# Kernel tuning notes

Measured on AMD Instinct MI355X. Metric: run time of the kernel, lower is better.

Reference implementation:

```python
import jax, jax.numpy as jnp
import numpy as np

N_NODES = 100000
N_EDGES = 1600000
IN_DIM, HID_DIM, OUT_DIM = 128, 64, 64


def setup_inputs() -> dict:
    key = jax.random.key(0)
    ks = jax.random.split(key, 12)
    x = jax.random.normal(ks[0], (N_NODES, IN_DIM), dtype=jnp.float32)
    src = jax.random.randint(ks[1], (N_EDGES,), 0, N_NODES, dtype=jnp.int32)
    dst = jax.random.randint(ks[2], (N_EDGES,), 0, N_NODES, dtype=jnp.int32)
    def glorot(k, shape):
        lim = float(np.sqrt(6.0 / (shape[0] + shape[1])))
        return jax.random.uniform(k, shape, jnp.float32, -lim, lim)
    W0 = glorot(ks[3], (IN_DIM, HID_DIM)); b0 = jnp.zeros((HID_DIM,), jnp.float32)
    W1 = glorot(ks[4], (HID_DIM, HID_DIM)); b1 = jnp.zeros((HID_DIM,), jnp.float32)
    W2 = glorot(ks[5], (HID_DIM, OUT_DIM)); b2 = jnp.zeros((OUT_DIM,), jnp.float32)
    Wl = glorot(ks[6], (OUT_DIM, OUT_DIM)); bl = jnp.zeros((OUT_DIM,), jnp.float32)
    return {"x": x, "src": src, "dst": dst,
            "W0": W0, "b0": b0, "W1": W1, "b1": b1,
            "W2": W2, "b2": b2, "Wl": Wl, "bl": bl}


def _graph_conv(x, src, dst, W, b, inv_sqrt_out, inv_sqrt_in):
    # DGL GraphConv, norm='both': D_out^{-1/2} then XW, SpMM aggregate, D_in^{-1/2}, +bias
    h = x * inv_sqrt_out[:, None]          # [N, d_in]
    h = h @ W                               # [N, d_out] (project first: d_in >= d_out)
    agg = jax.ops.segment_sum(h[src], dst, num_segments=N_NODES)  # gather+scatter over edges
    return agg * inv_sqrt_in[:, None] + b


def reference(x, src, dst, W0, b0, W1, b1, W2, b2, Wl, bl):
    ones_e = jnp.ones((N_EDGES,), jnp.float32)
    deg_out = jnp.clip(jax.ops.segment_sum(ones_e, src, num_segments=N_NODES), 1.0)
    deg_in = jnp.clip(jax.ops.segment_sum(ones_e, dst, num_segments=N_NODES), 1.0)
    inv_out = jax.lax.rsqrt(deg_out)
    inv_in = jax.lax.rsqrt(deg_in)
    h = jax.nn.elu(_graph_conv(x, src, dst, W0, b0, inv_out, inv_in))
    h = jax.nn.elu(_graph_conv(h, src, dst, W1, b1, inv_out, inv_in))
    h = _graph_conv(h, src, dst, W2, b2, inv_out, inv_in)
    return jax.nn.elu(h) @ Wl + bl
```

## Files before the change

kernel.cpp:

```cpp
#include <hip/hip_runtime.h>
#include <hip/hip_fp16.h>
#include <cstdint>
#include <cstddef>


#define WG 256
static constexpr int NCHUNK = 512;
static constexpr int RW_SH  = 7;
static constexpr int RWID   = 1 << RW_SH;
static constexpr int BPRO   = 12512;
static constexpr int NRO    = 8;
static constexpr int NCO    = 40;

typedef _Float16 half8 __attribute__((ext_vector_type(8)));
typedef _Float16 half2v __attribute__((ext_vector_type(2)));
typedef float f32x4 __attribute__((ext_vector_type(4)));

__device__ __forceinline__ int block_scan_excl(int v, int tid, int* sd, int& total) {
  sd[tid] = v;
  __syncthreads();
  for (int off = 1; off < 256; off <<= 1) {
    int t = (tid >= off) ? sd[tid - off] : 0;
    __syncthreads();
    sd[tid] += t;
    __syncthreads();
  }
  int incl = sd[tid];
  total = sd[255];
  __syncthreads();
  return incl - v;
}

__global__ __launch_bounds__(WG) void coarse_hist_kernel(const int* __restrict__ dst,
                                                         int* __restrict__ cntA,
                                                         int NR, int E, int EPC) {
  __shared__ int cnt[1024];
  const int c = blockIdx.x, tid = threadIdx.x;
  for (int i = tid; i < NR; i += WG) cnt[i] = 0;
  __syncthreads();
  const int base = c * EPC;
  const int nv4 = EPC >> 2;
  const int4* d4 = (const int4*)(dst + base);
  for (int i = tid; i < nv4; i += WG) {
    const int e = base + (i << 2);
    if (e + 3 < E) {
      const int4 v = d4[i];
      atomicAdd(&cnt[v.x >> RW_SH], 1);
      atomicAdd(&cnt[v.y >> RW_SH], 1);
      atomicAdd(&cnt[v.z >> RW_SH], 1);
      atomicAdd(&cnt[v.w >> RW_SH], 1);
    } else {
      for (int j = 0; j < 4; ++j) {
        const int ee = e + j;
        if (ee < E) atomicAdd(&cnt[dst[ee] >> RW_SH], 1);
      }
    }
  }
  __syncthreads();
  for (int i = tid; i < NR; i += WG) cntA[i * NCHUNK + c] = cnt[i];
}

__global__ __launch_bounds__(WG) void chunkscan_kernel(const int* __restrict__ cntA,
                                                       int* __restrict__ base_rel,
                                                       int* __restrict__ cntR) {
  __shared__ int sd[256];
  const int r = blockIdx.x, tid = threadIdx.x;
  const int row = r * NCHUNK;
  int t0, t1;
  const int v0 = cntA[row + tid];
  const int e0 = block_scan_excl(v0, tid, sd, t0);
  base_rel[row + tid] = e0;
  const int v1 = cntA[row + 256 + tid];
  const int e1 = block_scan_excl(v1, tid, sd, t1);
  base_rel[row + 256 + tid] = t0 + e1;
  if (tid == 0) cntR[r] = t0 + t1;
}

__global__ __launch_bounds__(WG) void rangescan_kernel(const int* __restrict__ cntR,
                                                       int* __restrict__ rangeStart,
                                                       int* __restrict__ rptr,
                                                       int NR, int N, int E) {
  __shared__ int sd[256];
  const int tid = threadIdx.x;
  int carry = 0;
  for (int base = 0; base < NR; base += 256) {
    const int idx = base + tid;
    const int v = (idx < NR) ? cntR[idx] : 0;
    int tot;
    const int e = block_scan_excl(v, tid, sd, tot);
    if (idx < NR) rangeStart[idx] = carry + e;
    carry += tot;
  }
  if (tid == 0) { rangeStart[NR] = E; rptr[N] = E; }
}

__global__ __launch_bounds__(WG) void bucket_kernel(const int* __restrict__ src,
                                                    const int* __restrict__ dst,
                                                    const int* __restrict__ base_rel,
                                                    const int* __restrict__ rangeStart,
                                                    int* __restrict__ bucket,
                                                    int NR, int E, int EPC) {
  __shared__ int cur[1024];
  const int c = blockIdx.x, tid = threadIdx.x;
  for (int i = tid; i < NR; i += WG) cur[i] = rangeStart[i] + base_rel[i * NCHUNK + c];
  __syncthreads();
  const int base = c * EPC;
  const int nv4 = EPC >> 2;
  const int4* s4 = (const int4*)(src + base);
  const int4* d4 = (const int4*)(dst + base);
  for (int i = tid; i < nv4; i += WG) {
    const int e = base + (i << 2);
    if (e + 3 < E) {
      const int4 sv = s4[i];
      const int4 dv = d4[i];
      int p;
      p = atomicAdd(&cur[dv.x >> RW_SH], 1); bucket[p] = (sv.x << RW_SH) | (dv.x & (RWID - 1));
      p = atomicAdd(&cur[dv.y >> RW_SH], 1); bucket[p] = (sv.y << RW_SH) | (dv.y & (RWID - 1));
      p = atomicAdd(&cur[dv.z >> RW_SH], 1); bucket[p] = (sv.z << RW_SH) | (dv.z & (RWID - 1));
      p = atomicAdd(&cur[dv.w >> RW_SH], 1); bucket[p] = (sv.w << RW_SH) | (dv.w & (RWID - 1));
    } else {
      for (int j = 0; j < 4; ++j) {
        const int ee = e + j;
        if (ee < E) {
          const int s = src[ee], d = dst[ee];
          const int p = atomicAdd(&cur[d >> RW_SH], 1);
          bucket[p] = (s << RW_SH) | (d & (RWID - 1));
        }
      }
    }
  }
}

__global__ __launch_bounds__(WG) void csr_kernel(const int* __restrict__ bucket,
                                                 const int* __restrict__ rangeStart,
                                                 int* __restrict__ rptr,
                                                 int* __restrict__ degi,
                                                 int* __restrict__ esrc, int N) {
  __shared__ int hist[RWID], sd[256];
  const int r = blockIdx.x, tid = threadIdx.x;
  const int s0 = rangeStart[r], s1 = rangeStart[r + 1];
  if (tid < RWID) hist[tid] = 0;
  __syncthreads();
  for (int e = s0 + tid; e < s1; e += WG) atomicAdd(&hist[bucket[e] & (RWID - 1)], 1);
  __syncthreads();
  const int v = (tid < RWID) ? hist[tid] : 0;
  int tot;
  const int excl = block_scan_excl(v, tid, sd, tot);
  const int node = (r << RW_SH) + tid;
  if (tid < RWID && node < N) { degi[node] = v; rptr[node] = s0 + excl; }
  if (tid < RWID) hist[tid] = s0 + excl;
  __syncthreads();
  for (int e = s0 + tid; e < s1; e += WG) {
    const int pk = bucket[e];
    const int p = atomicAdd(&hist[pk & (RWID - 1)], 1);
    esrc[p] = pk >> RW_SH;
  }
}

__global__ __launch_bounds__(WG) void dego_hist_kernel(const int* __restrict__ src,
                                                       int* __restrict__ slab,
                                                       int N, int E, int EPCO) {
  __shared__ int h[BPRO / 2];
  const int rr = blockIdx.x / NCO, cc = blockIdx.x % NCO;
  const int tid = threadIdx.x;
  for (int i = tid; i < (BPRO >> 3); i += WG) ((int4*)h)[i] = make_int4(0, 0, 0, 0);
  __syncthreads();
  const int lo = rr * BPRO;
  const int base = cc * EPCO;
  const int nv4 = EPCO >> 2;
  const int4* s4 = (const int4*)(src + base);
  for (int i = tid; i < nv4; i += WG) {
    const int e = base + (i << 2);
    if (e + 3 < E) {
      const int4 v = s4[i];
      unsigned b;
      b = (unsigned)(v.x - lo); if (b < (unsigned)BPRO) atomicAdd((unsigned*)&h[b >> 1], 1u << ((b & 1) << 4));
      b = (unsigned)(v.y - lo); if (b < (unsigned)BPRO) atomicAdd((unsigned*)&h[b >> 1], 1u << ((b & 1) << 4));
      b = (unsigned)(v.z - lo); if (b < (unsigned)BPRO) atomicAdd((unsigned*)&h[b >> 1], 1u << ((b & 1) << 4));
      b = (unsigned)(v.w - lo); if (b < (unsigned)BPRO) atomicAdd((unsigned*)&h[b >> 1], 1u << ((b & 1) << 4));
    } else {
      for (int j = 0; j < 4; ++j) {
        const int ee = e + j;
        if (ee < E) {
          const unsigned b = (unsigned)(src[ee] - lo);
          if (b < (unsigned)BPRO) atomicAdd((unsigned*)&h[b >> 1], 1u << ((b & 1) << 4));
        }
      }
    }
  }
  __syncthreads();
  const int NW = N >> 1;
  const int wbase = lo >> 1;
  int* srow = slab + (size_t)cc * NW;
  for (int i = tid; i < (BPRO >> 3); i += WG) {
    const int wg = wbase + (i << 2);
    if (wg + 3 < NW) {
      ((int4*)(srow + wg))[0] = ((const int4*)h)[i];
    } else {
      for (int j = 0; j < 4; ++j)
        if (wg + j < NW) srow[wg + j] = h[(i << 2) + j];
    }
  }
}

__global__ __launch_bounds__(WG) void dego_reduce_inv_kernel(const int* __restrict__ slab,
                                                             const int* __restrict__ degi,
                                                             float* __restrict__ invo,
                                                             float* __restrict__ invi, int N) {
  const int NW = N >> 1;
  const int i = blockIdx.x * WG + threadIdx.x;
  if (i >= NW) return;
  unsigned s = 0;
#pragma unroll
  for (int c = 0; c < NCO; ++c) s += (unsigned)slab[(size_t)c * NW + i];
  int d0 = (int)(s & 0xffffu); if (d0 < 1) d0 = 1;
  int d1 = (int)(s >> 16);     if (d1 < 1) d1 = 1;
  const int2 dd = *(const int2*)(degi + 2 * i);
  const int i0 = (dd.x < 1) ? 1 : dd.x;
  const int i1 = (dd.y < 1) ? 1 : dd.y;
  *(float2*)(invo + 2 * i) = make_float2(rsqrtf((float)d0), rsqrtf((float)d1));
  *(float2*)(invi + 2 * i) = make_float2(rsqrtf((float)i0), rsqrtf((float)i1));
}

__global__ __launch_bounds__(WG) void wtrans_kernel(const float* __restrict__ W0,
                                                    const float* __restrict__ W1,
                                                    const float* __restrict__ W2,
                                                    const float* __restrict__ Wl,
                                                    _Float16* __restrict__ T0,
                                                    _Float16* __restrict__ T1,
                                                    _Float16* __restrict__ T2,
                                                    _Float16* __restrict__ Tl) {
  const float* W; _Float16* T; int K;
  switch (blockIdx.x) {
    case 0: W = W0; T = T0; K = 128; break;
    case 1: W = W1; T = T1; K = 64; break;
    case 2: W = W2; T = T2; K = 64; break;
    default: W = Wl; T = Tl; K = 64; break;
  }
  for (int i = threadIdx.x; i < K * 64; i += WG) {
    const int k = i >> 6, c = i & 63;
    T[c * K + k] = (_Float16)W[i];
  }
}

template <int K, bool F16IN>
__global__ __launch_bounds__(256) void gemm_conv_mfma(const void* __restrict__ inv_,
                                                      const _Float16* __restrict__ WT,
                                                      const float* __restrict__ invo,
                                                      _Float16* __restrict__ hP, int N) {
  const int tid = threadIdx.x;
  const int w = tid >> 6, l = tid & 63;
  const int rowA = blockIdx.x * 64 + w * 16 + (l & 15);
  const int ar = (rowA < N) ? rowA : (N - 1);
  const int g8 = (l >> 4) * 8;

  f32x4 acc[4];
#pragma unroll
  for (int t = 0; t < 4; ++t) acc[t] = (f32x4){0.f, 0.f, 0.f, 0.f};

#pragma unroll
  for (int s = 0; s < K / 32; ++s) {
    const int kb = s * 32 + g8;
    half8 a;
    if constexpr (F16IN) {
      a = *(const half8*)((const _Float16*)inv_ + (size_t)ar * K + kb);
    } else {
      const float* in = (const float*)inv_;
      const float4 f0 = *(const float4*)(in + (size_t)ar * K + kb);
      const float4 f1 = *(const float4*)(in + (size_t)ar * K + kb + 4);
      a[0] = (_Float16)f0.x; a[1] = (_Float16)f0.y; a[2] = (_Float16)f0.z; a[3] = (_Float16)f0.w;
      a[4] = (_Float16)f1.x; a[5] = (_Float16)f1.y; a[6] = (_Float16)f1.z; a[7] = (_Float16)f1.w;
    }
#pragma unroll
    for (int t = 0; t < 4; ++t) {
      const half8 b = *(const half8*)(WT + (size_t)(16 * t + (l & 15)) * K + kb);
      acc[t] = __builtin_amdgcn_mfma_f32_16x16x32_f16(a, b, acc[t], 0, 0, 0);
    }
  }

  const int rbase = blockIdx.x * 64 + w * 16 + (l >> 4) * 4;
#pragma unroll
  for (int r = 0; r < 4; ++r) {
    const int row = rbase + r;
    if (row < N) {
      const float sc = invo[row];
#pragma unroll
      for (int t = 0; t < 4; ++t)
        hP[(size_t)row * 64 + 16 * t + (l & 15)] = (_Float16)(acc[t][r] * sc);
    }
  }
}

__global__ __launch_bounds__(256) void gemm_head_mfma(const _Float16* __restrict__ in,
                                                      const _Float16* __restrict__ WT,
                                                      const float* __restrict__ bias,
                                                      float* __restrict__ out, int N) {
  constexpr int K = 64;
  const int tid = threadIdx.x;
  const int w = tid >> 6, l = tid & 63;
  const int rowA = blockIdx.x * 64 + w * 16 + (l & 15);
  const int ar = (rowA < N) ? rowA : (N - 1);
  const int g8 = (l >> 4) * 8;

  f32x4 acc[4];
#pragma unroll
  for (int t = 0; t < 4; ++t) acc[t] = (f32x4){0.f, 0.f, 0.f, 0.f};

#pragma unroll
  for (int s = 0; s < K / 32; ++s) {
    const int kb = s * 32 + g8;
    const half8 a = *(const half8*)(in + (size_t)ar * K + kb);
#pragma unroll
    for (int t = 0; t < 4; ++t) {
      const half8 b = *(const half8*)(WT + (size_t)(16 * t + (l & 15)) * K + kb);
      acc[t] = __builtin_amdgcn_mfma_f32_16x16x32_f16(a, b, acc[t], 0, 0, 0);
    }
  }

  const int rbase = blockIdx.x * 64 + w * 16 + (l >> 4) * 4;
#pragma unroll
  for (int r = 0; r < 4; ++r) {
    const int row = rbase + r;
    if (row < N) {
#pragma unroll
      for (int t = 0; t < 4; ++t) {
        const int c = 16 * t + (l & 15);
        out[(size_t)row * 64 + c] = acc[t][r] + bias[c];
      }
    }
  }
}

__global__ __launch_bounds__(256) void agg_kernel(const _Float16* __restrict__ hp,
                                                  const int* __restrict__ rptr,
                                                  const int* __restrict__ esrc,
                                                  const float* __restrict__ invin,
                                                  const float* __restrict__ bias,
                                                  _Float16* __restrict__ out, int N,
                                                  int apply_elu) {
  const int w = (blockIdx.x * 256 + threadIdx.x) >> 6;
  const int lane = threadIdx.x & 63;
  const int g = lane >> 3;
  const int f8 = lane & 7;
  if (w >= N) return;
  const int e0 = rptr[w];
  const int e1 = rptr[w + 1];
  const int f = f8 * 8 + g;
  const float vi = invin[w];
  const float bv = bias[f];

  float acc[8];
#pragma unroll
  for (int k = 0; k < 8; ++k) acc[k] = 0.f;

  int e = e0;
  for (; e + 16 <= e1; e += 16) {
    const int sA = esrc[e + g];
    const int sB = esrc[e + 8 + g];
    const half8 hA8 = *(const half8*)(hp + (size_t)sA * 64 + f8 * 8);
    const half8 hB8 = *(const half8*)(hp + (size_t)sB * 64 + f8 * 8);
#if __has_builtin(__builtin_amdgcn_fdot2)
    const half2v one2 = {(_Float16)1.0f, (_Float16)1.0f};
#pragma unroll
    for (int k = 0; k < 8; ++k) {
      half2v p; p[0] = hA8[k]; p[1] = hB8[k];
      acc[k] = __builtin_amdgcn_fdot2(p, one2, acc[k], false);
    }
#else
#pragma unroll
    for (int k = 0; k < 8; ++k) acc[k] += (float)hA8[k] + (float)hB8[k];
#endif
  }
  for (; e + 8 <= e1; e += 8) {
    const int s = esrc[e + g];
    const half8 hv = *(const half8*)(hp + (size_t)s * 64 + f8 * 8);
#pragma unroll
    for (int k = 0; k < 8; ++k) acc[k] += (float)hv[k];
  }
  if (e < e1) {
    const int rem = e1 - e;
    int idx = e + g; if (idx > e1 - 1) idx = e1 - 1;
    const int s = esrc[idx];
    const half8 hv = *(const half8*)(hp + (size_t)s * 64 + f8 * 8);
    const float m = (g < rem) ? 1.f : 0.f;
#pragma unroll
    for (int k = 0; k < 8; ++k) acc[k] = fmaf(m, (float)hv[k], acc[k]);
  }

  const bool gb0 = (g & 1) != 0;
  const float s0 = gb0 ? acc[0] : acc[1];
  const float s1 = gb0 ? acc[2] : acc[3];
  const float s2 = gb0 ? acc[4] : acc[5];
  const float s3 = gb0 ? acc[6] : acc[7];
  const float k0 = (gb0 ? acc[1] : acc[0]) + __shfl_xor(s0, 8);
  const float k1 = (gb0 ? acc[3] : acc[2]) + __shfl_xor(s1, 8);
  const float k2 = (gb0 ? acc[5] : acc[4]) + __shfl_xor(s2, 8);
  const float k3 = (gb0 ? acc[7] : acc[6]) + __shfl_xor(s3, 8);
  const bool gb1 = (g & 2) != 0;
  const float t0 = gb1 ? k0 : k1;
  const float t1 = gb1 ? k2 : k3;
  const float m0 = (gb1 ? k1 : k0) + __shfl_xor(t0, 16);
  const float m1 = (gb1 ? k3 : k2) + __shfl_xor(t1, 16);
  const bool gb2 = (g & 4) != 0;
  const float u0 = gb2 ? m0 : m1;
  float v = (gb2 ? m1 : m0) + __shfl_xor(u0, 32);

  v = v * vi + bv;
  if (apply_elu) v = (v > 0.f) ? v : (__expf(v) - 1.0f);
  out[(size_t)w * 64 + f] = (_Float16)v;
}

extern "C" void kernel_launch(void* const* d_in, const int* in_sizes, int n_in,
                              void* d_out, int out_size, void* d_ws, size_t ws_size,
                              hipStream_t stream) {
  const float* x  = (const float*)d_in[0];
  const int*   src = (const int*)d_in[1];
  const int*   dst = (const int*)d_in[2];
  const float* W0 = (const float*)d_in[3];
  const float* b0 = (const float*)d_in[4];
  const float* W1 = (const float*)d_in[5];
  const float* b1 = (const float*)d_in[6];
  const float* W2 = (const float*)d_in[7];
  const float* b2 = (const float*)d_in[8];
  const float* Wl = (const float*)d_in[9];
  const float* bl = (const float*)d_in[10];

  const int N = in_sizes[0] / 128;
  const int E = in_sizes[1];
  const int NR = (N + RWID - 1) >> RW_SH;
  const int EPC = (((E + NCHUNK - 1) / NCHUNK) + 3) & ~3;
  const int EPCO = (((E + NCO - 1) / NCO) + 3) & ~3;

  int* wsp = (int*)d_ws;
  size_t off = 0;
  auto alloc = [&](size_t n) -> int* {
    int* p = wsp + off;
    off += (n + 63) & ~(size_t)63;
    return p;
  };
  int*      degi       = alloc(N);
  float*    invo       = (float*)alloc(N);
  float*    invi       = (float*)alloc(N);
  int*      rptr       = alloc((size_t)N + 1);
  int*      esrc       = alloc(E);
  int*      cntA       = alloc((size_t)NR * NCHUNK);
  int*      base_rel   = alloc((size_t)NR * NCHUNK);
  int*      cntR       = alloc(NR);
  int*      rangeStart = alloc((size_t)NR + 1);
  int*      bucket     = alloc(E);
  int*      slab       = alloc((size_t)NCO * (N >> 1));
  _Float16* hP         = (_Float16*)alloc((size_t)N * 32);
  _Float16* hA         = (_Float16*)alloc((size_t)N * 32);
  _Float16* WT0        = (_Float16*)alloc(64 * 128 / 2);
  _Float16* WT1        = (_Float16*)alloc(64 * 64 / 2);
  _Float16* WT2        = (_Float16*)alloc(64 * 64 / 2);
  _Float16* WTl        = (_Float16*)alloc(64 * 64 / 2);
  (void)ws_size; (void)n_in; (void)out_size;

  const int gAgg = (N + 3) / 4;
  const int gGemm = (N + 63) / 64;
  const int gRed = ((N >> 1) + WG - 1) / WG;

  coarse_hist_kernel<<<NCHUNK, WG, 0, stream>>>(dst, cntA, NR, E, EPC);
  chunkscan_kernel<<<NR, WG, 0, stream>>>(cntA, base_rel, cntR);
  rangescan_kernel<<<1, WG, 0, stream>>>(cntR, rangeStart, rptr, NR, N, E);
  bucket_kernel<<<NCHUNK, WG, 0, stream>>>(src, dst, base_rel, rangeStart, bucket, NR, E, EPC);
  csr_kernel<<<NR, WG, 0, stream>>>(bucket, rangeStart, rptr, degi, esrc, N);

  dego_hist_kernel<<<NRO * NCO, WG, 0, stream>>>(src, slab, N, E, EPCO);
  dego_reduce_inv_kernel<<<gRed, WG, 0, stream>>>(slab, degi, invo, invi, N);
  wtrans_kernel<<<4, WG, 0, stream>>>(W0, W1, W2, Wl, WT0, WT1, WT2, WTl);

  gemm_conv_mfma<128, false><<<gGemm, 256, 0, stream>>>(x, WT0, invo, hP, N);
  agg_kernel<<<gAgg, 256, 0, stream>>>(hP, rptr, esrc, invi, b0, hA, N, 1);
  gemm_conv_mfma<64, true><<<gGemm, 256, 0, stream>>>(hA, WT1, invo, hP, N);
  agg_kernel<<<gAgg, 256, 0, stream>>>(hP, rptr, esrc, invi, b1, hA, N, 1);
  gemm_conv_mfma<64, true><<<gGemm, 256, 0, stream>>>(hA, WT2, invo, hP, N);
  agg_kernel<<<gAgg, 256, 0, stream>>>(hP, rptr, esrc, invi, b2, hA, N, 1);
  gemm_head_mfma<<<gGemm, 256, 0, stream>>>(hA, WTl, bl, (float*)d_out, N);
}
```

Baseline: 264.5 us.

## Aggregate four destination nodes per wavefront and widen out-degree histogram slabs

The SpMM aggregation kernel now gives each wavefront four consecutive destination nodes instead of one. Their edge loops are interleaved so more independent gathers are in flight per wave, and the grid shrinks fourfold. The cost is higher register pressure, predicated loads when node degrees differ, and fewer waves overall. Separately, the out-degree histogram slab count grows from 40 to 64 to spread its atomic contention further, at the cost of a larger reduction.

After: 279.2 us. 1.06x slower.

```diff
diff --git a/kernel.cpp b/kernel.cpp
--- a/kernel.cpp
+++ b/kernel.cpp
@@ -10,7 +10,7 @@
 static constexpr int RWID   = 1 << RW_SH;
 static constexpr int BPRO   = 12512;
 static constexpr int NRO    = 8;
-static constexpr int NCO    = 40;
+static constexpr int NCO    = 64;
 
 typedef _Float16 half8 __attribute__((ext_vector_type(8)));
 typedef _Float16 half2v __attribute__((ext_vector_type(2)));
@@ -331,62 +331,7 @@
   }
 }
 
-__global__ __launch_bounds__(256) void agg_kernel(const _Float16* __restrict__ hp,
-                                                  const int* __restrict__ rptr,
-                                                  const int* __restrict__ esrc,
-                                                  const float* __restrict__ invin,
-                                                  const float* __restrict__ bias,
-                                                  _Float16* __restrict__ out, int N,
-                                                  int apply_elu) {
-  const int w = (blockIdx.x * 256 + threadIdx.x) >> 6;
-  const int lane = threadIdx.x & 63;
-  const int g = lane >> 3;
-  const int f8 = lane & 7;
-  if (w >= N) return;
-  const int e0 = rptr[w];
-  const int e1 = rptr[w + 1];
-  const int f = f8 * 8 + g;
-  const float vi = invin[w];
-  const float bv = bias[f];
-
-  float acc[8];
-#pragma unroll
-  for (int k = 0; k < 8; ++k) acc[k] = 0.f;
-
-  int e = e0;
-  for (; e + 16 <= e1; e += 16) {
-    const int sA = esrc[e + g];
-    const int sB = esrc[e + 8 + g];
-    const half8 hA8 = *(const half8*)(hp + (size_t)sA * 64 + f8 * 8);
-    const half8 hB8 = *(const half8*)(hp + (size_t)sB * 64 + f8 * 8);
-#if __has_builtin(__builtin_amdgcn_fdot2)
-    const half2v one2 = {(_Float16)1.0f, (_Float16)1.0f};
-#pragma unroll
-    for (int k = 0; k < 8; ++k) {
-      half2v p; p[0] = hA8[k]; p[1] = hB8[k];
-      acc[k] = __builtin_amdgcn_fdot2(p, one2, acc[k], false);
-    }
-#else
-#pragma unroll
-    for (int k = 0; k < 8; ++k) acc[k] += (float)hA8[k] + (float)hB8[k];
-#endif
-  }
-  for (; e + 8 <= e1; e += 8) {
-    const int s = esrc[e + g];
-    const half8 hv = *(const half8*)(hp + (size_t)s * 64 + f8 * 8);
-#pragma unroll
-    for (int k = 0; k < 8; ++k) acc[k] += (float)hv[k];
-  }
-  if (e < e1) {
-    const int rem = e1 - e;
-    int idx = e + g; if (idx > e1 - 1) idx = e1 - 1;
-    const int s = esrc[idx];
-    const half8 hv = *(const half8*)(hp + (size_t)s * 64 + f8 * 8);
-    const float m = (g < rem) ? 1.f : 0.f;
-#pragma unroll
-    for (int k = 0; k < 8; ++k) acc[k] = fmaf(m, (float)hv[k], acc[k]);
-  }
-
+__device__ __forceinline__ float reduce_scatter8(const float* acc, int g) {
   const bool gb0 = (g & 1) != 0;
   const float s0 = gb0 ? acc[0] : acc[1];
   const float s1 = gb0 ? acc[2] : acc[3];
@@ -403,11 +348,108 @@
   const float m1 = (gb1 ? k3 : k2) + __shfl_xor(t1, 16);
   const bool gb2 = (g & 4) != 0;
   const float u0 = gb2 ? m0 : m1;
-  float v = (gb2 ? m1 : m0) + __shfl_xor(u0, 32);
-
-  v = v * vi + bv;
-  if (apply_elu) v = (v > 0.f) ? v : (__expf(v) - 1.0f);
-  out[(size_t)w * 64 + f] = (_Float16)v;
+  return (gb2 ? m1 : m0) + __shfl_xor(u0, 32);
+}
+
+__global__ __launch_bounds__(256) void agg_kernel4(const _Float16* __restrict__ hp,
+                                                   const int* __restrict__ rptr,
+                                                   const int* __restrict__ esrc,
+                                                   const float* __restrict__ invin,
+                                                   const float* __restrict__ bias,
+                                                   _Float16* __restrict__ out, int N,
+                                                   int apply_elu) {
+  const int wv = (blockIdx.x * 256 + threadIdx.x) >> 6;
+  const int lane = threadIdx.x & 63;
+  const int g = lane >> 3;
+  const int f8 = lane & 7;
+  const int nb = wv * 4;
+  if (nb >= N) return;
+  const int f = f8 * 8 + g;
+  const float bv = bias[f];
+
+  const int i1 = (nb + 1 < N) ? nb + 1 : N;
+  const int i2 = (nb + 2 < N) ? nb + 2 : N;
+  const int i3 = (nb + 3 < N) ? nb + 3 : N;
+  const int i4 = (nb + 4 < N) ? nb + 4 : N;
+  int lo0 = rptr[nb], lo1 = rptr[i1], lo2 = rptr[i2], lo3 = rptr[i3];
+  const int hi0 = lo1, hi1 = lo2, hi2 = lo3, hi3 = rptr[i4];
+
+  float acc0[8] = {0}, acc1[8] = {0}, acc2[8] = {0}, acc3[8] = {0};
+
+#if __has_builtin(__builtin_amdgcn_fdot2)
+  const half2v one2 = {(_Float16)1.0f, (_Float16)1.0f};
+#define ACCPAIR(A_, X_, Y_) do { _Pragma("unroll") \
+  for (int k = 0; k < 8; ++k) { half2v p; p[0] = X_[k]; p[1] = Y_[k]; \
+    A_[k] = __builtin_amdgcn_fdot2(p, one2, A_[k], false); } } while (0)
+#else
+#define ACCPAIR(A_, X_, Y_) do { _Pragma("unroll") \
+  for (int k = 0; k < 8; ++k) A_[k] += (float)X_[k] + (float)Y_[k]; } while (0)
+#endif
+#define ACCONE(A_, X_) do { _Pragma("unroll") \
+  for (int k = 0; k < 8; ++k) A_[k] += (float)X_[k]; } while (0)
+#define GPAIR(lo_, XA_, XB_) do { \
+  const int sA_ = esrc[(lo_) + g], sB_ = esrc[(lo_) + 8 + g]; \
+  XA_ = *(const half8*)(hp + (size_t)sA_ * 64 + f8 * 8); \
+  XB_ = *(const half8*)(hp + (size_t)sB_ * 64 + f8 * 8); } while (0)
+
+  while (true) {
+    const bool a0 = lo0 + 16 <= hi0;
+    const bool a1 = lo1 + 16 <= hi1;
+    const bool a2 = lo2 + 16 <= hi2;
+    const bool a3 = lo3 + 16 <= hi3;
+    if (!(a0 | a1 | a2 | a3)) break;
+    half8 A0, B0, A1, B1, A2, B2, A3, B3;
+    if (a0) GPAIR(lo0, A0, B0);
+    if (a1) GPAIR(lo1, A1, B1);
+    if (a2) GPAIR(lo2, A2, B2);
+    if (a3) GPAIR(lo3, A3, B3);
+    if (a0) { ACCPAIR(acc0, A0, B0); lo0 += 16; }
+    if (a1) { ACCPAIR(acc1, A1, B1); lo1 += 16; }
+    if (a2) { ACCPAIR(acc2, A2, B2); lo2 += 16; }
+    if (a3) { ACCPAIR(acc3, A3, B3); lo3 += 16; }
+  }
+
+  {
+    const bool c0 = lo0 + 8 <= hi0;
+    const bool c1 = lo1 + 8 <= hi1;
+    const bool c2 = lo2 + 8 <= hi2;
+    const bool c3 = lo3 + 8 <= hi3;
+    half8 A0, A1, A2, A3;
+    if (c0) { const int s = esrc[lo0 + g]; A0 = *(const half8*)(hp + (size_t)s * 64 + f8 * 8); }
+    if (c1) { const int s = esrc[lo1 + g]; A1 = *(const half8*)(hp + (size_t)s * 64 + f8 * 8); }
+    if (c2) { const int s = esrc[lo2 + g]; A2 = *(const half8*)(hp + (size_t)s * 64 + f8 * 8); }
+    if (c3) { const int s = esrc[lo3 + g]; A3 = *(const half8*)(hp + (size_t)s * 64 + f8 * 8); }
+    if (c0) { ACCONE(acc0, A0); lo0 += 8; }
+    if (c1) { ACCONE(acc1, A1); lo1 += 8; }
+    if (c2) { ACCONE(acc2, A2); lo2 += 8; }
+    if (c3) { ACCONE(acc3, A3); lo3 += 8; }
+  }
+
+#define TAIL(lo_, hi_, A_) do { if ((lo_) < (hi_)) { \
+    const int rem_ = (hi_) - (lo_); \
+    int idx_ = (lo_) + g; if (idx_ > (hi_) - 1) idx_ = (hi_) - 1; \
+    const int s_ = esrc[idx_]; \
+    const half8 hv_ = *(const half8*)(hp + (size_t)s_ * 64 + f8 * 8); \
+    const float m_ = (g < rem_) ? 1.f : 0.f; \
+    _Pragma("unroll") for (int k = 0; k < 8; ++k) A_[k] = fmaf(m_, (float)hv_[k], A_[k]); } } while (0)
+  TAIL(lo0, hi0, acc0);
+  TAIL(lo1, hi1, acc1);
+  TAIL(lo2, hi2, acc2);
+  TAIL(lo3, hi3, acc3);
+#undef TAIL
+#undef GPAIR
+#undef ACCONE
+#undef ACCPAIR
+
+#define EPI(J_, A_) do { const int node_ = nb + (J_); if (node_ < N) { \
+    float v_ = reduce_scatter8(A_, g) * invin[node_] + bv; \
+    if (apply_elu) v_ = (v_ > 0.f) ? v_ : (__expf(v_) - 1.0f); \
+    out[(size_t)node_ * 64 + f] = (_Float16)v_; } } while (0)
+  EPI(0, acc0);
+  EPI(1, acc1);
+  EPI(2, acc2);
+  EPI(3, acc3);
+#undef EPI
 }
 
 extern "C" void kernel_launch(void* const* d_in, const int* in_sizes, int n_in,
@@ -457,7 +499,7 @@
   _Float16* WTl        = (_Float16*)alloc(64 * 64 / 2);
   (void)ws_size; (void)n_in; (void)out_size;
 
-  const int gAgg = (N + 3) / 4;
+  const int gAgg = (N + 15) / 16;
   const int gGemm = (N + 63) / 64;
   const int gRed = ((N >> 1) + WG - 1) / WG;
 
@@ -472,10 +514,10 @@
   wtrans_kernel<<<4, WG, 0, stream>>>(W0, W1, W2, Wl, WT0, WT1, WT2, WTl);
 
   gemm_conv_mfma<128, false><<<gGemm, 256, 0, stream>>>(x, WT0, invo, hP, N);
-  agg_kernel<<<gAgg, 256, 0, stream>>>(hP, rptr, esrc, invi, b0, hA, N, 1);
+  agg_kernel4<<<gAgg, 256, 0, stream>>>(hP, rptr, esrc, invi, b0, hA, N, 1);
   gemm_conv_mfma<64, true><<<gGemm, 256, 0, stream>>>(hA, WT1, invo, hP, N);
-  agg_kernel<<<gAgg, 256, 0, stream>>>(hP, rptr, esrc, invi, b1, hA, N, 1);
+  agg_kernel4<<<gAgg, 256, 0, stream>>>(hP, rptr, esrc, invi, b1, hA, N, 1);
   gemm_conv_mfma<64, true><<<gGemm, 256, 0, stream>>>(hA, WT2, invo, hP, N);
-  agg_kernel<<<gAgg, 256, 0, stream>>>(hP, rptr, esrc, invi, b2, hA, N, 1);
+  agg_kernel4<<<gAgg, 256, 0, stream>>>(hP, rptr, esrc, invi, b2, hA, N, 1);
   gemm_head_mfma<<<gGemm, 256, 0, stream>>>(hA, WTl, bl, (float*)d_out, N);
 }
```

## Merge independent setup kernels into two multi-role launches and fold invi into CSR

Applied to the files above, without the earlier changes.

Merges the coarse dst histogram, out-degree histogram and weight transpose into one launch whose blocks take different roles by block index. A second launch pairs the chunk scan with the out-degree reduction. The in-degree inverse sqrt is now computed inside the CSR kernel, which removes the degi buffer and the separate reduce kernel. The out-degree slab split grows from 40 to 64 chunks to give more parallel blocks. The aim is to cut launch count and let independent setup work overlap, at the cost of more slab rows to reduce and heterogeneous blocks sharing one grid.

Result: faster. 242.9 us (-8.2%).

```diff
diff --git a/kernel.cpp b/kernel.cpp
--- a/kernel.cpp
+++ b/kernel.cpp
@@ -10,7 +10,7 @@
 static constexpr int RWID   = 1 << RW_SH;
 static constexpr int BPRO   = 12512;
 static constexpr int NRO    = 8;
-static constexpr int NCO    = 40;
+static constexpr int NCO    = 64;
 
 typedef _Float16 half8 __attribute__((ext_vector_type(8)));
 typedef _Float16 half2v __attribute__((ext_vector_type(2)));
@@ -31,49 +31,138 @@
   return incl - v;
 }
 
-__global__ __launch_bounds__(WG) void coarse_hist_kernel(const int* __restrict__ dst,
-                                                         int* __restrict__ cntA,
-                                                         int NR, int E, int EPC) {
-  __shared__ int cnt[1024];
-  const int c = blockIdx.x, tid = threadIdx.x;
-  for (int i = tid; i < NR; i += WG) cnt[i] = 0;
-  __syncthreads();
-  const int base = c * EPC;
-  const int nv4 = EPC >> 2;
-  const int4* d4 = (const int4*)(dst + base);
-  for (int i = tid; i < nv4; i += WG) {
-    const int e = base + (i << 2);
-    if (e + 3 < E) {
-      const int4 v = d4[i];
-      atomicAdd(&cnt[v.x >> RW_SH], 1);
-      atomicAdd(&cnt[v.y >> RW_SH], 1);
-      atomicAdd(&cnt[v.z >> RW_SH], 1);
-      atomicAdd(&cnt[v.w >> RW_SH], 1);
-    } else {
-      for (int j = 0; j < 4; ++j) {
-        const int ee = e + j;
-        if (ee < E) atomicAdd(&cnt[dst[ee] >> RW_SH], 1);
+__global__ __launch_bounds__(WG) void setup1_kernel(const int* __restrict__ src,
+                                                    const int* __restrict__ dst,
+                                                    int* __restrict__ cntA,
+                                                    int* __restrict__ slab,
+                                                    const float* __restrict__ W0,
+                                                    const float* __restrict__ W1,
+                                                    const float* __restrict__ W2,
+                                                    const float* __restrict__ Wl,
+                                                    _Float16* __restrict__ T0,
+                                                    _Float16* __restrict__ T1,
+                                                    _Float16* __restrict__ T2,
+                                                    _Float16* __restrict__ Tl,
+                                                    int NR, int N, int E, int EPC, int EPCO) {
+  __shared__ int smem[BPRO / 2];
+  const int b = blockIdx.x, tid = threadIdx.x;
+
+  if (b < NCHUNK) {
+    int* cnt = smem;
+    for (int i = tid; i < NR; i += WG) cnt[i] = 0;
+    __syncthreads();
+    const int base = b * EPC;
+    const int nv4 = EPC >> 2;
+    const int4* d4 = (const int4*)(dst + base);
+    for (int i = tid; i < nv4; i += WG) {
+      const int e = base + (i << 2);
+      if (e + 3 < E) {
+        const int4 v = d4[i];
+        atomicAdd(&cnt[v.x >> RW_SH], 1);
+        atomicAdd(&cnt[v.y >> RW_SH], 1);
+        atomicAdd(&cnt[v.z >> RW_SH], 1);
+        atomicAdd(&cnt[v.w >> RW_SH], 1);
+      } else {
+        for (int j = 0; j < 4; ++j) {
+          const int ee = e + j;
+          if (ee < E) atomicAdd(&cnt[dst[ee] >> RW_SH], 1);
+        }
       }
     }
-  }
-  __syncthreads();
-  for (int i = tid; i < NR; i += WG) cntA[i * NCHUNK + c] = cnt[i];
-}
-
-__global__ __launch_bounds__(WG) void chunkscan_kernel(const int* __restrict__ cntA,
-                                                       int* __restrict__ base_rel,
-                                                       int* __restrict__ cntR) {
+    __syncthreads();
+    for (int i = tid; i < NR; i += WG) cntA[i * NCHUNK + b] = cnt[i];
+    return;
+  }
+
+  if (b < NCHUNK + NRO * NCO) {
+    int* h = smem;
+    const int bb = b - NCHUNK;
+    const int rr = bb / NCO, cc = bb % NCO;
+    for (int i = tid; i < (BPRO >> 3); i += WG) ((int4*)h)[i] = make_int4(0, 0, 0, 0);
+    __syncthreads();
+    const int lo = rr * BPRO;
+    const int base = cc * EPCO;
+    const int nv4 = EPCO >> 2;
+    const int4* s4 = (const int4*)(src + base);
+    for (int i = tid; i < nv4; i += WG) {
+      const int e = base + (i << 2);
+      if (e + 3 < E) {
+        const int4 v = s4[i];
+        unsigned x;
+        x = (unsigned)(v.x - lo); if (x < (unsigned)BPRO) atomicAdd((unsigned*)&h[x >> 1], 1u << ((x & 1) << 4));
+        x = (unsigned)(v.y - lo); if (x < (unsigned)BPRO) atomicAdd((unsigned*)&h[x >> 1], 1u << ((x & 1) << 4));
+        x = (unsigned)(v.z - lo); if (x < (unsigned)BPRO) atomicAdd((unsigned*)&h[x >> 1], 1u << ((x & 1) << 4));
+        x = (unsigned)(v.w - lo); if (x < (unsigned)BPRO) atomicAdd((unsigned*)&h[x >> 1], 1u << ((x & 1) << 4));
+      } else {
+        for (int j = 0; j < 4; ++j) {
+          const int ee = e + j;
+          if (ee < E) {
+            const unsigned x = (unsigned)(src[ee] - lo);
+            if (x < (unsigned)BPRO) atomicAdd((unsigned*)&h[x >> 1], 1u << ((x & 1) << 4));
+          }
+        }
+      }
+    }
+    __syncthreads();
+    const int NW = N >> 1;
+    const int wbase = lo >> 1;
+    int* srow = slab + (size_t)cc * NW;
+    for (int i = tid; i < (BPRO >> 3); i += WG) {
+      const int wg = wbase + (i << 2);
+      if (wg + 3 < NW) {
+        ((int4*)(srow + wg))[0] = ((const int4*)h)[i];
+      } else {
+        for (int j = 0; j < 4; ++j)
+          if (wg + j < NW) srow[wg + j] = h[(i << 2) + j];
+      }
+    }
+    return;
+  }
+
+  const float* W; _Float16* T; int K;
+  switch (b - (NCHUNK + NRO * NCO)) {
+    case 0: W = W0; T = T0; K = 128; break;
+    case 1: W = W1; T = T1; K = 64; break;
+    case 2: W = W2; T = T2; K = 64; break;
+    default: W = Wl; T = Tl; K = 64; break;
+  }
+  for (int i = tid; i < K * 64; i += WG) {
+    const int k = i >> 6, c = i & 63;
+    T[c * K + k] = (_Float16)W[i];
+  }
+}
+
+__global__ __launch_bounds__(WG) void setup2_kernel(const int* __restrict__ cntA,
+                                                    int* __restrict__ base_rel,
+                                                    int* __restrict__ cntR,
+                                                    const int* __restrict__ slab,
+                                                    float* __restrict__ invo,
+                                                    int NR, int N) {
   __shared__ int sd[256];
-  const int r = blockIdx.x, tid = threadIdx.x;
-  const int row = r * NCHUNK;
-  int t0, t1;
-  const int v0 = cntA[row + tid];
-  const int e0 = block_scan_excl(v0, tid, sd, t0);
-  base_rel[row + tid] = e0;
-  const int v1 = cntA[row + 256 + tid];
-  const int e1 = block_scan_excl(v1, tid, sd, t1);
-  base_rel[row + 256 + tid] = t0 + e1;
-  if (tid == 0) cntR[r] = t0 + t1;
+  const int b = blockIdx.x, tid = threadIdx.x;
+
+  if (b < NR) {
+    const int row = b * NCHUNK;
+    int t0, t1;
+    const int v0 = cntA[row + tid];
+    const int e0 = block_scan_excl(v0, tid, sd, t0);
+    base_rel[row + tid] = e0;
+    const int v1 = cntA[row + 256 + tid];
+    const int e1 = block_scan_excl(v1, tid, sd, t1);
+    base_rel[row + 256 + tid] = t0 + e1;
+    if (tid == 0) cntR[b] = t0 + t1;
+    return;
+  }
+
+  const int NW = N >> 1;
+  const int i = (b - NR) * WG + tid;
+  if (i >= NW) return;
+  unsigned s = 0;
+#pragma unroll
+  for (int c = 0; c < NCO; ++c) s += (unsigned)slab[(size_t)c * NW + i];
+  int d0 = (int)(s & 0xffffu); if (d0 < 1) d0 = 1;
+  int d1 = (int)(s >> 16);     if (d1 < 1) d1 = 1;
+  *(float2*)(invo + 2 * i) = make_float2(rsqrtf((float)d0), rsqrtf((float)d1));
 }
 
 __global__ __launch_bounds__(WG) void rangescan_kernel(const int* __restrict__ cntR,
@@ -134,7 +223,7 @@
 __global__ __launch_bounds__(WG) void csr_kernel(const int* __restrict__ bucket,
                                                  const int* __restrict__ rangeStart,
                                                  int* __restrict__ rptr,
-                                                 int* __restrict__ degi,
+                                                 float* __restrict__ invi,
                                                  int* __restrict__ esrc, int N) {
   __shared__ int hist[RWID], sd[256];
   const int r = blockIdx.x, tid = threadIdx.x;
@@ -147,99 +236,16 @@
   int tot;
   const int excl = block_scan_excl(v, tid, sd, tot);
   const int node = (r << RW_SH) + tid;
-  if (tid < RWID && node < N) { degi[node] = v; rptr[node] = s0 + excl; }
+  if (tid < RWID && node < N) {
+    rptr[node] = s0 + excl;
+    invi[node] = rsqrtf((float)((v < 1) ? 1 : v));
+  }
   if (tid < RWID) hist[tid] = s0 + excl;
   __syncthreads();
   for (int e = s0 + tid; e < s1; e += WG) {
     const int pk = bucket[e];
     const int p = atomicAdd(&hist[pk & (RWID - 1)], 1);
     esrc[p] = pk >> RW_SH;
-  }
-}
-
-__global__ __launch_bounds__(WG) void dego_hist_kernel(const int* __restrict__ src,
-                                                       int* __restrict__ slab,
-                                                       int N, int E, int EPCO) {
-  __shared__ int h[BPRO / 2];
-  const int rr = blockIdx.x / NCO, cc = blockIdx.x % NCO;
-  const int tid = threadIdx.x;
-  for (int i = tid; i < (BPRO >> 3); i += WG) ((int4*)h)[i] = make_int4(0, 0, 0, 0);
-  __syncthreads();
-  const int lo = rr * BPRO;
-  const int base = cc * EPCO;
-  const int nv4 = EPCO >> 2;
-  const int4* s4 = (const int4*)(src + base);
-  for (int i = tid; i < nv4; i += WG) {
-    const int e = base + (i << 2);
-    if (e + 3 < E) {
-      const int4 v = s4[i];
-      unsigned b;
-      b = (unsigned)(v.x - lo); if (b < (unsigned)BPRO) atomicAdd((unsigned*)&h[b >> 1], 1u << ((b & 1) << 4));
-      b = (unsigned)(v.y - lo); if (b < (unsigned)BPRO) atomicAdd((unsigned*)&h[b >> 1], 1u << ((b & 1) << 4));
-      b = (unsigned)(v.z - lo); if (b < (unsigned)BPRO) atomicAdd((unsigned*)&h[b >> 1], 1u << ((b & 1) << 4));
-      b = (unsigned)(v.w - lo); if (b < (unsigned)BPRO) atomicAdd((unsigned*)&h[b >> 1], 1u << ((b & 1) << 4));
-    } else {
-      for (int j = 0; j < 4; ++j) {
-        const int ee = e + j;
-        if (ee < E) {
-          const unsigned b = (unsigned)(src[ee] - lo);
-          if (b < (unsigned)BPRO) atomicAdd((unsigned*)&h[b >> 1], 1u << ((b & 1) << 4));
-        }
-      }
-    }
-  }
-  __syncthreads();
-  const int NW = N >> 1;
-  const int wbase = lo >> 1;
-  int* srow = slab + (size_t)cc * NW;
-  for (int i = tid; i < (BPRO >> 3); i += WG) {
-    const int wg = wbase + (i << 2);
-    if (wg + 3 < NW) {
-      ((int4*)(srow + wg))[0] = ((const int4*)h)[i];
-    } else {
-      for (int j = 0; j < 4; ++j)
-        if (wg + j < NW) srow[wg + j] = h[(i << 2) + j];
-    }
-  }
-}
-
-__global__ __launch_bounds__(WG) void dego_reduce_inv_kernel(const int* __restrict__ slab,
-                                                             const int* __restrict__ degi,
-                                                             float* __restrict__ invo,
-                                                             float* __restrict__ invi, int N) {
-  const int NW = N >> 1;
-  const int i = blockIdx.x * WG + threadIdx.x;
-  if (i >= NW) return;
-  unsigned s = 0;
-#pragma unroll
-  for (int c = 0; c < NCO; ++c) s += (unsigned)slab[(size_t)c * NW + i];
-  int d0 = (int)(s & 0xffffu); if (d0 < 1) d0 = 1;
-  int d1 = (int)(s >> 16);     if (d1 < 1) d1 = 1;
-  const int2 dd = *(const int2*)(degi + 2 * i);
-  const int i0 = (dd.x < 1) ? 1 : dd.x;
-  const int i1 = (dd.y < 1) ? 1 : dd.y;
-  *(float2*)(invo + 2 * i) = make_float2(rsqrtf((float)d0), rsqrtf((float)d1));
-  *(float2*)(invi + 2 * i) = make_float2(rsqrtf((float)i0), rsqrtf((float)i1));
-}
-
-__global__ __launch_bounds__(WG) void wtrans_kernel(const float* __restrict__ W0,
-                                                    const float* __restrict__ W1,
-                                                    const float* __restrict__ W2,
-                                                    const float* __restrict__ Wl,
-                                                    _Float16* __restrict__ T0,
-                                                    _Float16* __restrict__ T1,
-                                                    _Float16* __restrict__ T2,
-                                                    _Float16* __restrict__ Tl) {
-  const float* W; _Float16* T; int K;
-  switch (blockIdx.x) {
-    case 0: W = W0; T = T0; K = 128; break;
-    case 1: W = W1; T = T1; K = 64; break;
-    case 2: W = W2; T = T2; K = 64; break;
-    default: W = Wl; T = Tl; K = 64; break;
-  }
-  for (int i = threadIdx.x; i < K * 64; i += WG) {
-    const int k = i >> 6, c = i & 63;
-    T[c * K + k] = (_Float16)W[i];
   }
 }
 
@@ -438,7 +444,6 @@
     off += (n + 63) & ~(size_t)63;
     return p;
   };
-  int*      degi       = alloc(N);
   float*    invo       = (float*)alloc(N);
   float*    invi       = (float*)alloc(N);
   int*      rptr       = alloc((size_t)N + 1);
@@ -459,17 +464,14 @@
 
   const int gAgg = (N + 3) / 4;
   const int gGemm = (N + 63) / 64;
-  const int gRed = ((N >> 1) + WG - 1) / WG;
-
-  coarse_hist_kernel<<<NCHUNK, WG, 0, stream>>>(dst, cntA, NR, E, EPC);
-  chunkscan_kernel<<<NR, WG, 0, stream>>>(cntA, base_rel, cntR);
+  const int gInvo = ((N >> 1) + WG - 1) / WG;
+
+  setup1_kernel<<<NCHUNK + NRO * NCO + 4, WG, 0, stream>>>(
+      src, dst, cntA, slab, W0, W1, W2, Wl, WT0, WT1, WT2, WTl, NR, N, E, EPC, EPCO);
+  setup2_kernel<<<NR + gInvo, WG, 0, stream>>>(cntA, base_rel, cntR, slab, invo, NR, N);
   rangescan_kernel<<<1, WG, 0, stream>>>(cntR, rangeStart, rptr, NR, N, E);
   bucket_kernel<<<NCHUNK, WG, 0, stream>>>(src, dst, base_rel, rangeStart, bucket, NR, E, EPC);
-  csr_kernel<<<NR, WG, 0, stream>>>(bucket, rangeStart, rptr, degi, esrc, N);
-
-  dego_hist_kernel<<<NRO * NCO, WG, 0, stream>>>(src, slab, N, E, EPCO);
-  dego_reduce_inv_kernel<<<gRed, WG, 0, stream>>>(slab, degi, invo, invi, N);
-  wtrans_kernel<<<4, WG, 0, stream>>>(W0, W1, W2, Wl, WT0, WT1, WT2, WTl);
+  csr_kernel<<<NR, WG, 0, stream>>>(bucket, rangeStart, rptr, invi, esrc, N);
 
   gemm_conv_mfma<128, false><<<gGemm, 256, 0, stream>>>(x, WT0, invo, hP, N);
   agg_kernel<<<gAgg, 256, 0, stream>>>(hP, rptr, esrc, invi, b0, hA, N, 1);
```
